# Kernel optimization log

Measured on AMD Instinct MI355X. Metric: run time of the kernel, lower is better.

## Reference

```python
import jax, jax.numpy as jnp
import numpy as np
from jax import lax

B, L, ENC_IN, MARK = 8, 512, 7, 4
D_MODEL, EXPAND, D_STATE, D_CONV = 512, 2, 16, 4
D_INNER = D_MODEL * EXPAND
DT_RANK = int(np.ceil(D_MODEL / 16))  # 32
PRED_LEN, C_OUT = 96, 7


def _positional_embedding(seq_len, d_model):
    pos = jnp.arange(seq_len, dtype=jnp.float32)[:, None]
    div = jnp.exp(jnp.arange(0, d_model, 2, dtype=jnp.float32) * (-np.log(10000.0) / d_model))
    pe = jnp.zeros((seq_len, d_model), dtype=jnp.float32)
    pe = pe.at[:, 0::2].set(jnp.sin(pos * div))
    pe = pe.at[:, 1::2].set(jnp.cos(pos * div))
    return pe  # [L, d_model]


def setup_inputs() -> dict:
    key = jax.random.key(0)
    ks = jax.random.split(key, 20)
    s = 0.02
    inp = {
        "x_enc": jax.random.normal(ks[0], (B, L, ENC_IN), jnp.float32),
        "x_mark_enc": jax.random.normal(ks[1], (B, L, MARK), jnp.float32),
        "x_dec": jax.random.normal(ks[2], (B, 144, ENC_IN), jnp.float32),
        "x_mark_dec": jax.random.normal(ks[3], (B, 144, MARK), jnp.float32),
        # DataEmbedding params
        "token_conv_w": jax.random.normal(ks[4], (D_MODEL, ENC_IN, 3), jnp.float32) * s,
        "temporal_w": jax.random.normal(ks[5], (D_MODEL, MARK), jnp.float32) * s,
        # Mamba params
        "in_proj_w": jax.random.normal(ks[6], (2 * D_INNER, D_MODEL), jnp.float32) * s,
        "conv1d_w": jax.random.normal(ks[7], (D_INNER, 1, D_CONV), jnp.float32) * s,
        "conv1d_b": jnp.zeros((D_INNER,), jnp.float32),
        "x_proj_w": jax.random.normal(ks[8], (DT_RANK + 2 * D_STATE, D_INNER), jnp.float32) * s,
        "dt_proj_w": jax.random.normal(ks[9], (D_INNER, DT_RANK), jnp.float32) * s,
        "dt_proj_b": jax.random.normal(ks[10], (D_INNER,), jnp.float32) * s,
        "A_log": jnp.log(jnp.broadcast_to(jnp.arange(1, D_STATE + 1, dtype=jnp.float32), (D_INNER, D_STATE))),
        "D_param": jnp.ones((D_INNER,), jnp.float32),
        "out_proj_w": jax.random.normal(ks[11], (D_MODEL, D_INNER), jnp.float32) * s,
        # prediction head
        "head_w": jax.random.normal(ks[12], (PRED_LEN * C_OUT, D_MODEL), jnp.float32) * s,
        "head_b": jnp.zeros((PRED_LEN * C_OUT,), jnp.float32),
    }
    return inp


def reference(x_enc, x_mark_enc, x_dec, x_mark_dec, token_conv_w, temporal_w,
              in_proj_w, conv1d_w, conv1d_b, x_proj_w, dt_proj_w, dt_proj_b,
              A_log, D_param, out_proj_w, head_w, head_b):
    # --- instance normalization (mean/std detached as in torch) ---
    mean_enc = lax.stop_gradient(jnp.mean(x_enc, axis=1, keepdims=True))       # [B,1,C]
    xc = x_enc - mean_enc
    std_enc = lax.stop_gradient(jnp.sqrt(jnp.var(xc, axis=1, keepdims=True) + 1e-5))
    xn = xc / std_enc                                                          # [B,L,C]

    # --- DataEmbedding: circular conv token emb + timeF linear + sinusoidal PE ---
    xp = jnp.pad(xn, ((0, 0), (1, 1), (0, 0)), mode="wrap")                    # circular pad on L
    val = lax.conv_general_dilated(xp.transpose(0, 2, 1), token_conv_w, (1,), "VALID")  # [B,D,L]
    val = val.transpose(0, 2, 1)                                               # [B,L,D]
    temp = x_mark_enc @ temporal_w.T                                           # [B,L,D]
    x = val + temp + _positional_embedding(L, D_MODEL)[None]                   # [B,L,D]

    # --- Mamba block ---
    xz = x @ in_proj_w.T                                                       # [B,L,2*Di]
    x_part, z = jnp.split(xz, 2, axis=-1)
    # causal depthwise conv over time
    xt = jnp.pad(x_part.transpose(0, 2, 1), ((0, 0), (0, 0), (D_CONV - 1, 0)))
    xconv = lax.conv_general_dilated(xt, conv1d_w, (1,), "VALID",
                                     feature_group_count=D_INNER) + conv1d_b[None, :, None]
    u = jax.nn.silu(xconv.transpose(0, 2, 1))                                  # [B,L,Di]

    dbl = u @ x_proj_w.T                                                       # [B,L,dt_rank+2n]
    dt_low = dbl[..., :DT_RANK]
    Bm = dbl[..., DT_RANK:DT_RANK + D_STATE]                                   # [B,L,n]
    Cm = dbl[..., DT_RANK + D_STATE:]                                          # [B,L,n]
    dt = jax.nn.softplus(dt_low @ dt_proj_w.T + dt_proj_b)                     # [B,L,Di]

    A = -jnp.exp(A_log)                                                        # [Di,n]
    deltaA = jnp.exp(dt[..., None] * A)                                        # [B,L,Di,n]
    deltaBu = dt[..., None] * Bm[:, :, None, :] * u[..., None]                 # [B,L,Di,n]

    def step(h, inputs):
        dA_t, dBu_t, c_t = inputs                                              # [B,Di,n],[B,Di,n],[B,n]
        h = dA_t * h + dBu_t
        y_t = jnp.einsum("bdn,bn->bd", h, c_t)
        return h, y_t

    h0 = jnp.zeros((B, D_INNER, D_STATE), dtype=x.dtype)
    _, ys = lax.scan(step, h0, (deltaA.transpose(1, 0, 2, 3),
                                deltaBu.transpose(1, 0, 2, 3),
                                Cm.transpose(1, 0, 2)))
    y = ys.transpose(1, 0, 2) + u * D_param                                    # [B,L,Di]
    y = y * jax.nn.silu(z)
    x_out = y @ out_proj_w.T                                                   # [B,L,D]

    # --- prediction head on last hidden state ---
    last = x_out[:, -1, :]                                                     # [B,D]
    pred = (last @ head_w.T + head_b).reshape(-1, PRED_LEN, C_OUT)
    return pred * std_enc + mean_enc
```

## Files before the change

### kernel.cpp

```cpp
#include <hip/hip_runtime.h>
#include <hip/hip_bf16.h>
#include <math.h>

#define BB 8
#define LL 512
#define CIN 7
#define MARKN 4
#define DM 512
#define DI 1024
#define NOUTC 672
#define NTC 16

typedef unsigned short ushortT;
typedef __attribute__((ext_vector_type(8))) short short8v;
typedef __attribute__((ext_vector_type(4))) float f32x4;

__device__ __forceinline__ float bf2f(ushortT u){ return __uint_as_float(((unsigned)u)<<16); }
__device__ __forceinline__ ushortT f2bf(float f){ __hip_bfloat16 h = __float2bfloat16(f); return *(ushortT*)&h; }

__global__ __launch_bounds__(512) void k_prep_embed(const float* __restrict__ xe,
    const float* __restrict__ xmark, const float* __restrict__ tw,
    const float* __restrict__ tpw, const float* __restrict__ inprojw,
    const float* __restrict__ xpw,
    __hip_bfloat16* __restrict__ xo, ushortT* __restrict__ wbf,
    ushortT* __restrict__ xpwbf, float* __restrict__ mean, float* __restrict__ stdv){
  __shared__ float sw[DM*21];
  __shared__ float sxr[10][CIN];
  __shared__ float smr[8][MARKN];
  __shared__ float sMean[8], sInv[8];
  int blk = blockIdx.x, tid = threadIdx.x;
  if(blk < 512){
    int b = blk >> 6;
    int l0 = (blk & 63) << 3;
    int wv = tid >> 6, t2 = tid & 63;
    if(wv < 7){
      int c = wv;
      const float* base = xe + (b*LL)*CIN + c;
      float v[8]; float s = 0.f;
      #pragma unroll
      for(int i=0;i<8;i++){ v[i] = base[(t2 + i*64)*CIN]; s += v[i]; }
      #pragma unroll
      for(int o=32;o>=1;o>>=1) s += __shfl_down(s, o);
      float m = __shfl(s, 0) * (1.0f/LL);
      float vs = 0.f;
      #pragma unroll
      for(int i=0;i<8;i++){ float dv = v[i]-m; vs += dv*dv; }
      #pragma unroll
      for(int o=32;o>=1;o>>=1) vs += __shfl_down(vs, o);
      float var = __shfl(vs, 0) * (1.0f/LL);
      float sd = sqrtf(var + 1e-5f);
      if(t2 == 0){
        sMean[c] = m; sInv[c] = 1.0f/sd;
        if(l0 == 0){ mean[b*CIN+c] = m; stdv[b*CIN+c] = sd; }
      }
    }
    __syncthreads();
    for(int i=tid; i<DM*21; i+=512) sw[i] = tw[i];
    if(tid < 70){
      int r = tid / CIN, c = tid % CIN;
      int ls = (l0 - 1 + r + LL) % LL;
      sxr[r][c] = (xe[(b*LL + ls)*CIN + c] - sMean[c]) * sInv[c];
    } else if(tid >= 128 && tid < 160){
      int i2 = tid - 128; int r = i2 >> 2, m = i2 & 3;
      smr[r][m] = xmark[(b*LL + l0 + r)*MARKN + m];
    }
    __syncthreads();
    int d = tid;
    float wv2[21];
    #pragma unroll
    for(int i=0;i<21;i++) wv2[i] = sw[d*21 + i];
    float tv[4];
    #pragma unroll
    for(int m=0;m<4;m++) tv[m] = tpw[d*MARKN + m];
    float divv = expf((float)(2*(d>>1)) * (-0.0179889460390159843f));
    bool isodd = (d & 1) != 0;
    #pragma unroll
    for(int ll=0; ll<8; ll++){
      float acc = 0.f;
      #pragma unroll
      for(int c=0;c<CIN;c++){
        #pragma unroll
        for(int k=0;k<3;k++) acc += sxr[ll+k][c] * wv2[c*3+k];
      }
      #pragma unroll
      for(int m=0;m<4;m++) acc += smr[ll][m] * tv[m];
      float ang = (float)(l0+ll) * divv;
      acc += isodd ? cosf(ang) : sinf(ang);
      xo[(size_t)(b*LL + l0 + ll)*DM + d] = __float2bfloat16(acc);
    }
  } else if(blk < 1024){
    int i = ((blk-512)*512 + tid)*4;
    float4 v = *(const float4*)(inprojw + i);
    ushort4 pk; pk.x=f2bf(v.x); pk.y=f2bf(v.y); pk.z=f2bf(v.z); pk.w=f2bf(v.w);
    *(ushort4*)(wbf + i) = pk;
  } else {
    int i = ((blk-1024)*512 + tid)*4;
    float4 v = *(const float4*)(xpw + i);
    ushort4 pk; pk.x=f2bf(v.x); pk.y=f2bf(v.y); pk.z=f2bf(v.z); pk.w=f2bf(v.w);
    *(ushort4*)(xpwbf + i) = pk;
  }
}

__global__ __launch_bounds__(256) void k_inproj_mfma(const ushortT* __restrict__ A,
    const ushortT* __restrict__ Bw, ushortT* __restrict__ C){
  __shared__ ushortT Asl[2][128*64];
  __shared__ ushortT Bsl[2][128*64];
  int tid = threadIdx.x;
  int w = tid >> 6, l = tid & 63;
  int m0 = blockIdx.y * 128, n0 = blockIdx.x * 128;
  int wr = w >> 1, wc = w & 1;
  f32x4 acc[4][4] = {};
  int srow = l >> 3;
  int scolswz = ((l & 7) * 16) ^ (srow << 4);

#define IP_STAGE(bufi, kt) do{ \
    _Pragma("unroll") \
    for(int i=0;i<4;i++){ \
      int r0 = w*32 + i*8; \
      int r = r0 + srow; \
      const ushortT* gA = A + (size_t)(m0 + r)*512 + (kt)*64 + (scolswz>>1); \
      const ushortT* gB = Bw + (size_t)(n0 + r)*512 + (kt)*64 + (scolswz>>1); \
      __builtin_amdgcn_global_load_lds( \
        (const __attribute__((address_space(1))) unsigned int*)(const void*)gA, \
        (__attribute__((address_space(3))) unsigned int*)(void*)(Asl[bufi] + r0*64), 16, 0, 0); \
      __builtin_amdgcn_global_load_lds( \
        (const __attribute__((address_space(1))) unsigned int*)(const void*)gB, \
        (__attribute__((address_space(3))) unsigned int*)(void*)(Bsl[bufi] + r0*64), 16, 0, 0); \
    } }while(0)

  IP_STAGE(0, 0);
  __syncthreads();
  int cur = 0;
  for(int kt = 0; kt < 8; ++kt){
    if(kt < 7) IP_STAGE(cur^1, kt+1);
    #pragma unroll
    for(int kk=0;kk<2;kk++){
      short8v af[4], bfr[4];
      int cb = kk*64 + (l>>4)*16;
      #pragma unroll
      for(int mf=0;mf<4;mf++){
        int ar = wr*64 + mf*16 + (l&15);
        af[mf] = *(const short8v*)(Asl[cur] + ar*64 + ((cb ^ ((ar&7)<<4))>>1));
      }
      #pragma unroll
      for(int nf=0;nf<4;nf++){
        int br = wc*64 + nf*16 + (l&15);
        bfr[nf] = *(const short8v*)(Bsl[cur] + br*64 + ((cb ^ ((br&7)<<4))>>1));
      }
      #pragma unroll
      for(int mf=0;mf<4;mf++)
        #pragma unroll
        for(int nf=0;nf<4;nf++)
          acc[mf][nf] = __builtin_amdgcn_mfma_f32_16x16x32_bf16(af[mf], bfr[nf], acc[mf][nf], 0, 0, 0);
    }
    __syncthreads();
    cur ^= 1;
  }
#undef IP_STAGE
  #pragma unroll
  for(int mf=0;mf<4;mf++){
    int rbase = m0 + wr*64 + mf*16 + (l>>4)*4;
    #pragma unroll
    for(int nf=0;nf<4;nf++){
      int col = n0 + wc*64 + nf*16 + (l&15);
      #pragma unroll
      for(int r=0;r<4;r++)
        C[(size_t)(rbase+r)*1024 + col] = f2bf(acc[mf][nf][r]);
    }
  }
}

__global__ __launch_bounds__(1024) void k_dwconv(const ushortT* __restrict__ xpbf,
    const float* __restrict__ cw, const float* __restrict__ cb,
    ushortT* __restrict__ ubf){
  int blk = blockIdx.x;
  int b = blk >> 5, l0 = (blk & 31) * 16;
  int d = threadIdx.x;
  const float4 w4 = *(const float4*)(cw + d*4);
  float bias = cb[d];
  const ushortT* base = xpbf + (size_t)(b*LL + l0)*1024 + d;
  float x0=0.f, x1=0.f, x2=0.f;
  if(l0 > 0){
    x0 = bf2f(base[-3*1024]); x1 = bf2f(base[-2*1024]); x2 = bf2f(base[-1*1024]);
  }
  #pragma unroll
  for(int ll=0; ll<16; ++ll){
    float x3 = bf2f(base[(size_t)ll*1024]);
    float acc = bias + x0*w4.x + x1*w4.y + x2*w4.z + x3*w4.w;
    float s = acc / (1.f + __expf(-acc));
    ubf[(size_t)(b*LL + l0 + ll)*1024 + d] = f2bf(s);
    x0 = x1; x1 = x2; x2 = x3;
  }
}

__global__ __launch_bounds__(256) void k_xproj_mfma(const ushortT* __restrict__ A,
    const ushortT* __restrict__ Bw, float* __restrict__ C){
  __shared__ ushortT Asl[2][32*64];
  __shared__ ushortT Bsl[2][64*64];
  int tid = threadIdx.x;
  int w = tid >> 6, l = tid & 63;
  int m0 = blockIdx.x * 32;
  f32x4 acc[2] = {};
  int srow = l >> 3;
  int scol = ((l & 7) * 16) ^ (srow << 4);

#define XP_STAGE(bufi, kt) do{ \
    { \
      int r0 = w*8; \
      const ushortT* gA = A + (size_t)(m0 + r0 + srow)*1024 + (kt)*64 + (scol>>1); \
      __builtin_amdgcn_global_load_lds( \
        (const __attribute__((address_space(1))) unsigned int*)(const void*)gA, \
        (__attribute__((address_space(3))) unsigned int*)(void*)(Asl[bufi] + r0*64), 16, 0, 0); \
    } \
    _Pragma("unroll") \
    for(int i=0;i<2;i++){ \
      int r0 = w*16 + i*8; \
      const ushortT* gB = Bw + (size_t)(r0 + srow)*1024 + (kt)*64 + (scol>>1); \
      __builtin_amdgcn_global_load_lds( \
        (const __attribute__((address_space(1))) unsigned int*)(const void*)gB, \
        (__attribute__((address_space(3))) unsigned int*)(void*)(Bsl[bufi] + r0*64), 16, 0, 0); \
    } }while(0)

  XP_STAGE(0, 0);
  __syncthreads();
  int cur = 0;
  for(int kt = 0; kt < 16; ++kt){
    if(kt < 15) XP_STAGE(cur^1, kt+1);
    #pragma unroll
    for(int kk=0;kk<2;kk++){
      int cb = kk*64 + (l>>4)*16;
      int ar = (w&1)*16 + (l&15);
      short8v af = *(const short8v*)(Asl[cur] + ar*64 + ((cb ^ ((ar&7)<<4))>>1));
      #pragma unroll
      for(int nf=0;nf<2;nf++){
        int br = (w>>1)*32 + nf*16 + (l&15);
        short8v bfv = *(const short8v*)(Bsl[cur] + br*64 + ((cb ^ ((br&7)<<4))>>1));
        acc[nf] = __builtin_amdgcn_mfma_f32_16x16x32_bf16(af, bfv, acc[nf], 0, 0, 0);
      }
    }
    __syncthreads();
    cur ^= 1;
  }
#undef XP_STAGE
  int rbase = m0 + (w&1)*16 + (l>>4)*4;
  #pragma unroll
  for(int nf=0;nf<2;nf++){
    int col = (w>>1)*32 + nf*16 + (l&15);
    #pragma unroll
    for(int r=0;r<4;r++)
      C[(size_t)(rbase+r)*64 + col] = acc[nf][r];
  }
}

__global__ __launch_bounds__(256) void k_scan_chunk(const float* __restrict__ dbl,
    const ushortT* __restrict__ ubf, const float* __restrict__ dtw,
    const float* __restrict__ dtb, const float* __restrict__ alog,
    float4* __restrict__ P4, float4* __restrict__ Q4){
  int tc = blockIdx.x;
  int dgrp = blockIdx.y;
  int b = blockIdx.z;
  int tid = threadIdx.x;
  int d = dgrp*256 + tid;
  __shared__ float sD[32][68];
  #pragma unroll
  for(int j=0;j<2;j++){
    int idx = j*256 + tid;
    int row = idx >> 4, q = idx & 15;
    float4 v = *(const float4*)(dbl + (size_t)(b*LL + tc*32 + row)*64 + q*4);
    *(float4*)(&sD[row][q*4]) = v;
  }
  float wdt[32];
  #pragma unroll
  for(int r4=0;r4<8;r4++){
    float4 v = *(const float4*)(dtw + (size_t)d*32 + r4*4);
    wdt[r4*4]=v.x; wdt[r4*4+1]=v.y; wdt[r4*4+2]=v.z; wdt[r4*4+3]=v.w;
  }
  float bias = dtb[d];
  float Ad[16];
  {
    float4 a0 = *(const float4*)(alog + d*16);
    float4 a1 = *(const float4*)(alog + d*16 + 4);
    float4 a2 = *(const float4*)(alog + d*16 + 8);
    float4 a3 = *(const float4*)(alog + d*16 + 12);
    Ad[0]=-__expf(a0.x); Ad[1]=-__expf(a0.y); Ad[2]=-__expf(a0.z); Ad[3]=-__expf(a0.w);
    Ad[4]=-__expf(a1.x); Ad[5]=-__expf(a1.y); Ad[6]=-__expf(a1.z); Ad[7]=-__expf(a1.w);
    Ad[8]=-__expf(a2.x); Ad[9]=-__expf(a2.y); Ad[10]=-__expf(a2.z); Ad[11]=-__expf(a2.w);
    Ad[12]=-__expf(a3.x); Ad[13]=-__expf(a3.y); Ad[14]=-__expf(a3.z); Ad[15]=-__expf(a3.w);
  }
  __syncthreads();
  float h[16];
  #pragma unroll
  for(int n=0;n<16;n++) h[n] = 0.f;
  float Ss = 0.f;
  const ushortT* up = ubf + (size_t)(b*LL + tc*32)*1024 + d;
  #pragma unroll 2
  for(int t=0;t<32;t++){
    float a2 = bias;
    #pragma unroll
    for(int r=0;r<32;r++) a2 += sD[t][r]*wdt[r];
    float dtv = (a2 > 20.f) ? a2 : __logf(1.f + __expf(a2));
    float uv = bf2f(up[(size_t)t*1024]);
    float wt = dtv * uv;
    Ss += dtv;
    #pragma unroll
    for(int n=0;n<16;n++){
      float e = __expf(dtv * Ad[n]);
      h[n] = h[n]*e + wt*sD[t][32+n];
    }
  }
  size_t base4 = (size_t)(tc*8 + b)*4*1024 + d;
  #pragma unroll
  for(int n4=0;n4<4;n4++){
    Q4[base4 + n4*1024] = make_float4(h[n4*4], h[n4*4+1], h[n4*4+2], h[n4*4+3]);
    P4[base4 + n4*1024] = make_float4(__expf(Ss*Ad[n4*4]), __expf(Ss*Ad[n4*4+1]),
                                      __expf(Ss*Ad[n4*4+2]), __expf(Ss*Ad[n4*4+3]));
  }
}

__global__ __launch_bounds__(256) void k_scan_combine(const float4* __restrict__ P4,
    const float4* __restrict__ Q4, const float* __restrict__ dbl,
    const ushortT* __restrict__ ubf, const ushortT* __restrict__ xbf,
    const ushortT* __restrict__ wbf, const float* __restrict__ Dp,
    float* __restrict__ yv){
  int tid = threadIdx.x;
  int unit = blockIdx.x*64 + (tid>>2);
  int sub = tid & 3;
  int b = unit >> 10, d = unit & 1023;
  const ushortT* xr = xbf + (size_t)(b*LL + LL-1)*512 + sub*128;
  const ushortT* wr = wbf + (size_t)(1024 + d)*512 + sub*128;
  float zl = 0.f;
  #pragma unroll
  for(int k=0;k<128;k+=8){
    short8v xv = *(const short8v*)(xr + k);
    short8v wv = *(const short8v*)(wr + k);
    #pragma unroll
    for(int j=0;j<8;j++) zl += bf2f((ushortT)xv[j])*bf2f((ushortT)wv[j]);
  }
  zl += __shfl_xor(zl, 1);
  zl += __shfl_xor(zl, 2);
  float h0=0.f, h1=0.f, h2=0.f, h3=0.f;
  #pragma unroll
  for(int c=0;c<NTC;c++){
    size_t idx = (size_t)(c*8 + b)*4*1024 + sub*1024 + d;
    float4 pv = P4[idx];
    float4 qv = Q4[idx];
    h0 = pv.x*h0 + qv.x;
    h1 = pv.y*h1 + qv.y;
    h2 = pv.z*h2 + qv.z;
    h3 = pv.w*h3 + qv.w;
  }
  const float* Crow = dbl + (size_t)(b*LL + LL-1)*64 + 48 + sub*4;
  float y = Crow[0]*h0 + Crow[1]*h1 + Crow[2]*h2 + Crow[3]*h3;
  y += __shfl_xor(y, 1);
  y += __shfl_xor(y, 2);
  if(sub == 0){
    float ul = bf2f(ubf[(size_t)(b*LL + LL-1)*1024 + d]);
    float sz = zl / (1.f + __expf(-zl));
    yv[b*1024 + d] = (y + ul*Dp[d]) * sz;
  }
}

__global__ __launch_bounds__(256) void k_outproj(const float* __restrict__ yv,
    const float* __restrict__ W, float* __restrict__ xout){
  int tid = threadIdx.x;
  int j = blockIdx.x*8 + (tid>>5);
  int ks = tid & 31;
  float a[8] = {};
  #pragma unroll
  for(int t=0;t<8;t++){
    int k = ks*4 + t*128;
    float4 wv = *(const float4*)(W + (size_t)j*1024 + k);
    #pragma unroll
    for(int b=0;b<8;b++){
      float4 xv = *(const float4*)(yv + b*1024 + k);
      a[b] += xv.x*wv.x + xv.y*wv.y + xv.z*wv.z + xv.w*wv.w;
    }
  }
  #pragma unroll
  for(int b=0;b<8;b++){
    #pragma unroll
    for(int o=16;o>=1;o>>=1) a[b] += __shfl_xor(a[b], o);
  }
  if(ks==0){
    #pragma unroll
    for(int b=0;b<8;b++) xout[b*512 + j] = a[b];
  }
}

__global__ __launch_bounds__(256) void k_head(const float* __restrict__ xout,
    const float* __restrict__ W, const float* __restrict__ hb,
    const float* __restrict__ mean, const float* __restrict__ stdv,
    float* __restrict__ out){
  int tid = threadIdx.x;
  int o = blockIdx.x*8 + (tid>>5);
  int ks = tid & 31;
  float a[8] = {};
  #pragma unroll
  for(int t=0;t<4;t++){
    int k = ks*4 + t*128;
    float4 wv = *(const float4*)(W + (size_t)o*512 + k);
    #pragma unroll
    for(int b=0;b<8;b++){
      float4 xv = *(const float4*)(xout + b*512 + k);
      a[b] += xv.x*wv.x + xv.y*wv.y + xv.z*wv.z + xv.w*wv.w;
    }
  }
  #pragma unroll
  for(int b=0;b<8;b++){
    #pragma unroll
    for(int oo=16;oo>=1;oo>>=1) a[b] += __shfl_xor(a[b], oo);
  }
  if(ks==0){
    int c = o % 7;
    #pragma unroll
    for(int b=0;b<8;b++){
      float v = a[b] + hb[o];
      out[b*NOUTC + o] = v * stdv[b*CIN + c] + mean[b*CIN + c];
    }
  }
}

extern "C" void kernel_launch(void* const* d_in, const int* in_sizes, int n_in,
                              void* d_out, int out_size, void* d_ws, size_t ws_size,
                              hipStream_t stream) {
  const float* x_enc   = (const float*)d_in[0];
  const float* x_mark  = (const float*)d_in[1];
  const float* tconvw  = (const float*)d_in[4];
  const float* tempw   = (const float*)d_in[5];
  const float* inprojw = (const float*)d_in[6];
  const float* convw   = (const float*)d_in[7];
  const float* convb   = (const float*)d_in[8];
  const float* xprojw  = (const float*)d_in[9];
  const float* dtw     = (const float*)d_in[10];
  const float* dtb     = (const float*)d_in[11];
  const float* alog    = (const float*)d_in[12];
  const float* dpar    = (const float*)d_in[13];
  const float* outw    = (const float*)d_in[14];
  const float* headw   = (const float*)d_in[15];
  const float* headb   = (const float*)d_in[16];

  float* ws    = (float*)d_ws;
  float* mean  = ws;
  float* stdv  = ws + 64;
  ushortT* xbf = (ushortT*)(ws + 128);
  ushortT* wbf = (ushortT*)(ws + 1048704);
  ushortT* xpwbf=(ushortT*)(ws + 1572992);
  ushortT* xpbf= (ushortT*)(ws + 1605760);
  ushortT* ubf = (ushortT*)(ws + 3702912);
  float* dbl   = ws + 5800064;
  float4* P4   = (float4*)(ws + 6062208);
  float4* Q4   = (float4*)(ws + 8159360);
  float* yv    = ws + 10256512;
  float* xout  = ws + 10264704;
  float* out   = (float*)d_out;

  k_prep_embed<<<1056, 512, 0, stream>>>(x_enc, x_mark, tconvw, tempw, inprojw, xprojw,
                                         (__hip_bfloat16*)xbf, wbf, xpwbf, mean, stdv);
  k_inproj_mfma<<<dim3(8, 32), 256, 0, stream>>>(xbf, wbf, xpbf);
  k_dwconv<<<256, 1024, 0, stream>>>(xpbf, convw, convb, ubf);
  k_xproj_mfma<<<128, 256, 0, stream>>>(ubf, xpwbf, dbl);
  k_scan_chunk<<<dim3(NTC, 4, 8), 256, 0, stream>>>(dbl, ubf, dtw, dtb, alog, P4, Q4);
  k_scan_combine<<<128, 256, 0, stream>>>(P4, Q4, dbl, ubf, xbf, wbf, dpar, yv);
  k_outproj<<<64, 256, 0, stream>>>(yv, outw, xout);
  k_head  <<<84, 256, 0, stream>>>(xout, headw, headb, mean, stdv, out);
}
```

Before: 88.84 us.

## Fuse x_proj GEMM into chunked scan kernel via shared memory

Merges the x_proj MFMA GEMM and the chunk scan into one kernel. Each block (chunk, batch) with 1024 threads has its first 4 waves compute the 32x64 dbl tile into LDS, then all threads run the scan for their channel. The last C row is exported separately for the combine step. This removes a launch and the global round trip of dbl. The cost is that 12 of 16 waves sit idle during the GEMM, and the grid shrinks to 128 large blocks, which may lower occupancy for the scan.

```diff
diff --git a/kernel.cpp b/kernel.cpp
--- a/kernel.cpp
+++ b/kernel.cpp
@@ -193,82 +193,74 @@
   }
 }
 
-__global__ __launch_bounds__(256) void k_xproj_mfma(const ushortT* __restrict__ A,
-    const ushortT* __restrict__ Bw, float* __restrict__ C){
+__global__ __launch_bounds__(1024) void k_xscan(const ushortT* __restrict__ Aub,
+    const ushortT* __restrict__ Bw, const float* __restrict__ dtw,
+    const float* __restrict__ dtb, const float* __restrict__ alog,
+    float4* __restrict__ P4, float4* __restrict__ Q4, float* __restrict__ Crow){
+  int tc = blockIdx.x, b = blockIdx.y;
+  int tid = threadIdx.x;
   __shared__ ushortT Asl[2][32*64];
   __shared__ ushortT Bsl[2][64*64];
-  int tid = threadIdx.x;
-  int w = tid >> 6, l = tid & 63;
-  int m0 = blockIdx.x * 32;
+  __shared__ float sD[32][68];
+  int m0g = b*LL + tc*32;
   f32x4 acc[2] = {};
+  int w2 = (tid >> 6) & 3, l = tid & 63;
   int srow = l >> 3;
   int scol = ((l & 7) * 16) ^ (srow << 4);
-
-#define XP_STAGE(bufi, kt) do{ \
+  bool mfw = tid < 256;
+
+#define XS_STAGE(bufi, kt) do{ \
     { \
-      int r0 = w*8; \
-      const ushortT* gA = A + (size_t)(m0 + r0 + srow)*1024 + (kt)*64 + (scol>>1); \
+      int r0 = w2*8; \
+      const ushortT* gA = Aub + (size_t)(m0g + r0 + srow)*1024 + (kt)*64 + (scol>>1); \
       __builtin_amdgcn_global_load_lds( \
         (const __attribute__((address_space(1))) unsigned int*)(const void*)gA, \
         (__attribute__((address_space(3))) unsigned int*)(void*)(Asl[bufi] + r0*64), 16, 0, 0); \
     } \
     _Pragma("unroll") \
     for(int i=0;i<2;i++){ \
-      int r0 = w*16 + i*8; \
+      int r0 = w2*16 + i*8; \
       const ushortT* gB = Bw + (size_t)(r0 + srow)*1024 + (kt)*64 + (scol>>1); \
       __builtin_amdgcn_global_load_lds( \
         (const __attribute__((address_space(1))) unsigned int*)(const void*)gB, \
         (__attribute__((address_space(3))) unsigned int*)(void*)(Bsl[bufi] + r0*64), 16, 0, 0); \
     } }while(0)
 
-  XP_STAGE(0, 0);
+  if(mfw) XS_STAGE(0, 0);
   __syncthreads();
   int cur = 0;
   for(int kt = 0; kt < 16; ++kt){
-    if(kt < 15) XP_STAGE(cur^1, kt+1);
-    #pragma unroll
-    for(int kk=0;kk<2;kk++){
-      int cb = kk*64 + (l>>4)*16;
-      int ar = (w&1)*16 + (l&15);
-      short8v af = *(const short8v*)(Asl[cur] + ar*64 + ((cb ^ ((ar&7)<<4))>>1));
-      #pragma unroll
-      for(int nf=0;nf<2;nf++){
-        int br = (w>>1)*32 + nf*16 + (l&15);
-        short8v bfv = *(const short8v*)(Bsl[cur] + br*64 + ((cb ^ ((br&7)<<4))>>1));
-        acc[nf] = __builtin_amdgcn_mfma_f32_16x16x32_bf16(af, bfv, acc[nf], 0, 0, 0);
+    if(mfw){
+      if(kt < 15) XS_STAGE(cur^1, kt+1);
+      #pragma unroll
+      for(int kk=0;kk<2;kk++){
+        int cb = kk*64 + (l>>4)*16;
+        int ar = (w2&1)*16 + (l&15);
+        short8v af = *(const short8v*)(Asl[cur] + ar*64 + ((cb ^ ((ar&7)<<4))>>1));
+        #pragma unroll
+        for(int nf=0;nf<2;nf++){
+          int br = (w2>>1)*32 + nf*16 + (l&15);
+          short8v bfv = *(const short8v*)(Bsl[cur] + br*64 + ((cb ^ ((br&7)<<4))>>1));
+          acc[nf] = __builtin_amdgcn_mfma_f32_16x16x32_bf16(af, bfv, acc[nf], 0, 0, 0);
+        }
       }
     }
     __syncthreads();
     cur ^= 1;
   }
-#undef XP_STAGE
-  int rbase = m0 + (w&1)*16 + (l>>4)*4;
-  #pragma unroll
-  for(int nf=0;nf<2;nf++){
-    int col = (w>>1)*32 + nf*16 + (l&15);
-    #pragma unroll
-    for(int r=0;r<4;r++)
-      C[(size_t)(rbase+r)*64 + col] = acc[nf][r];
-  }
-}
-
-__global__ __launch_bounds__(256) void k_scan_chunk(const float* __restrict__ dbl,
-    const ushortT* __restrict__ ubf, const float* __restrict__ dtw,
-    const float* __restrict__ dtb, const float* __restrict__ alog,
-    float4* __restrict__ P4, float4* __restrict__ Q4){
-  int tc = blockIdx.x;
-  int dgrp = blockIdx.y;
-  int b = blockIdx.z;
-  int tid = threadIdx.x;
-  int d = dgrp*256 + tid;
-  __shared__ float sD[32][68];
-  #pragma unroll
-  for(int j=0;j<2;j++){
-    int idx = j*256 + tid;
-    int row = idx >> 4, q = idx & 15;
-    float4 v = *(const float4*)(dbl + (size_t)(b*LL + tc*32 + row)*64 + q*4);
-    *(float4*)(&sD[row][q*4]) = v;
-  }
+#undef XS_STAGE
+  if(mfw){
+    int rbase = (w2&1)*16 + (l>>4)*4;
+    #pragma unroll
+    for(int nf=0;nf<2;nf++){
+      int colx = (w2>>1)*32 + nf*16 + (l&15);
+      #pragma unroll
+      for(int r=0;r<4;r++) sD[rbase+r][colx] = acc[nf][r];
+    }
+  }
+  __syncthreads();
+  if(tc == 15 && tid < 16) Crow[b*16 + tid] = sD[31][48 + tid];
+  int d = tid;
   float wdt[32];
   #pragma unroll
   for(int r4=0;r4<8;r4++){
@@ -287,12 +279,11 @@
     Ad[8]=-__expf(a2.x); Ad[9]=-__expf(a2.y); Ad[10]=-__expf(a2.z); Ad[11]=-__expf(a2.w);
     Ad[12]=-__expf(a3.x); Ad[13]=-__expf(a3.y); Ad[14]=-__expf(a3.z); Ad[15]=-__expf(a3.w);
   }
-  __syncthreads();
   float h[16];
   #pragma unroll
   for(int n=0;n<16;n++) h[n] = 0.f;
   float Ss = 0.f;
-  const ushortT* up = ubf + (size_t)(b*LL + tc*32)*1024 + d;
+  const ushortT* up = Aub + (size_t)m0g*1024 + d;
   #pragma unroll 2
   for(int t=0;t<32;t++){
     float a2 = bias;
@@ -318,7 +309,7 @@
 }
 
 __global__ __launch_bounds__(256) void k_scan_combine(const float4* __restrict__ P4,
-    const float4* __restrict__ Q4, const float* __restrict__ dbl,
+    const float4* __restrict__ Q4, const float* __restrict__ Crow,
     const ushortT* __restrict__ ubf, const ushortT* __restrict__ xbf,
     const ushortT* __restrict__ wbf, const float* __restrict__ Dp,
     float* __restrict__ yv){
@@ -349,8 +340,8 @@
     h2 = pv.z*h2 + qv.z;
     h3 = pv.w*h3 + qv.w;
   }
-  const float* Crow = dbl + (size_t)(b*LL + LL-1)*64 + 48 + sub*4;
-  float y = Crow[0]*h0 + Crow[1]*h1 + Crow[2]*h2 + Crow[3]*h3;
+  const float* Cr = Crow + b*16 + sub*4;
+  float y = Cr[0]*h0 + Cr[1]*h1 + Cr[2]*h2 + Cr[3]*h3;
   y += __shfl_xor(y, 1);
   y += __shfl_xor(y, 2);
   if(sub == 0){
@@ -447,20 +438,19 @@
   ushortT* xpwbf=(ushortT*)(ws + 1572992);
   ushortT* xpbf= (ushortT*)(ws + 1605760);
   ushortT* ubf = (ushortT*)(ws + 3702912);
-  float* dbl   = ws + 5800064;
-  float4* P4   = (float4*)(ws + 6062208);
-  float4* Q4   = (float4*)(ws + 8159360);
-  float* yv    = ws + 10256512;
-  float* xout  = ws + 10264704;
+  float4* P4   = (float4*)(ws + 5800064);
+  float4* Q4   = (float4*)(ws + 7897216);
+  float* yv    = ws + 9994368;
+  float* xout  = ws + 10002560;
+  float* Crow  = ws + 10006656;
   float* out   = (float*)d_out;
 
   k_prep_embed<<<1056, 512, 0, stream>>>(x_enc, x_mark, tconvw, tempw, inprojw, xprojw,
                                          (__hip_bfloat16*)xbf, wbf, xpwbf, mean, stdv);
   k_inproj_mfma<<<dim3(8, 32), 256, 0, stream>>>(xbf, wbf, xpbf);
   k_dwconv<<<256, 1024, 0, stream>>>(xpbf, convw, convb, ubf);
-  k_xproj_mfma<<<128, 256, 0, stream>>>(ubf, xpwbf, dbl);
-  k_scan_chunk<<<dim3(NTC, 4, 8), 256, 0, stream>>>(dbl, ubf, dtw, dtb, alog, P4, Q4);
-  k_scan_combine<<<128, 256, 0, stream>>>(P4, Q4, dbl, ubf, xbf, wbf, dpar, yv);
+  k_xscan<<<dim3(NTC, 8), 1024, 0, stream>>>(ubf, xpwbf, dtw, dtb, alog, P4, Q4, Crow);
+  k_scan_combine<<<128, 256, 0, stream>>>(P4, Q4, Crow, ubf, xbf, wbf, dpar, yv);
   k_outproj<<<64, 256, 0, stream>>>(yv, outw, xout);
   k_head  <<<84, 256, 0, stream>>>(xout, headw, headb, mean, stdv, out);
 }
```

Result: slower. 98.99 us (+11.4%).

## Fuse depthwise causal conv and SiLU into in_proj GEMM epilogue with halo rows

Applied to the files above, without the earlier changes.

The in_proj GEMM now also computes 16 halo rows above each 128-row tile, so the causal depthwise conv plus SiLU can run directly from LDS in the epilogue. This removes the separate dwconv kernel launch and the global write and re-read of the bf16 x-projection intermediate. The cost is redundant halo MFMA work in two waves and a larger LDS footprint. The epilogue conv loop is also serialised at 64 rows per thread.

```diff
diff --git a/kernel.cpp b/kernel.cpp
--- a/kernel.cpp
+++ b/kernel.cpp
@@ -101,96 +101,117 @@
   }
 }
 
-__global__ __launch_bounds__(256) void k_inproj_mfma(const ushortT* __restrict__ A,
-    const ushortT* __restrict__ Bw, ushortT* __restrict__ C){
-  __shared__ ushortT Asl[2][128*64];
-  __shared__ ushortT Bsl[2][128*64];
+__global__ __launch_bounds__(256) void k_inproj_dw(const ushortT* __restrict__ A,
+    const ushortT* __restrict__ Bw, const float* __restrict__ cw,
+    const float* __restrict__ cb, ushortT* __restrict__ ubf){
+  __shared__ __align__(16) ushortT LDSI[2*144*64 + 2*128*64];
+#define ASLB(bufi) (LDSI + (bufi)*144*64)
+#define BSLB(bufi) (LDSI + 2*144*64 + (bufi)*128*64)
   int tid = threadIdx.x;
   int w = tid >> 6, l = tid & 63;
   int m0 = blockIdx.y * 128, n0 = blockIdx.x * 128;
   int wr = w >> 1, wc = w & 1;
+  int hbase = (m0 == 0) ? 0 : m0 - 16;
   f32x4 acc[4][4] = {};
+  f32x4 hacc[4] = {};
   int srow = l >> 3;
   int scolswz = ((l & 7) * 16) ^ (srow << 4);
 
-#define IP_STAGE(bufi, kt) do{ \
+#define IPD_STAGE(bufi, kt) do{ \
     _Pragma("unroll") \
     for(int i=0;i<4;i++){ \
       int r0 = w*32 + i*8; \
-      int r = r0 + srow; \
-      const ushortT* gA = A + (size_t)(m0 + r)*512 + (kt)*64 + (scolswz>>1); \
-      const ushortT* gB = Bw + (size_t)(n0 + r)*512 + (kt)*64 + (scolswz>>1); \
+      const ushortT* gA = A + (size_t)(m0 + r0 + srow)*512 + (kt)*64 + (scolswz>>1); \
+      const ushortT* gB = Bw + (size_t)(n0 + r0 + srow)*512 + (kt)*64 + (scolswz>>1); \
       __builtin_amdgcn_global_load_lds( \
         (const __attribute__((address_space(1))) unsigned int*)(const void*)gA, \
-        (__attribute__((address_space(3))) unsigned int*)(void*)(Asl[bufi] + r0*64), 16, 0, 0); \
+        (__attribute__((address_space(3))) unsigned int*)(void*)(ASLB(bufi) + (16 + r0)*64), 16, 0, 0); \
       __builtin_amdgcn_global_load_lds( \
         (const __attribute__((address_space(1))) unsigned int*)(const void*)gB, \
-        (__attribute__((address_space(3))) unsigned int*)(void*)(Bsl[bufi] + r0*64), 16, 0, 0); \
+        (__attribute__((address_space(3))) unsigned int*)(void*)(BSLB(bufi) + r0*64), 16, 0, 0); \
+    } \
+    if(w < 2){ \
+      int hr0 = w*8; \
+      const ushortT* gH = A + (size_t)(hbase + hr0 + srow)*512 + (kt)*64 + (scolswz>>1); \
+      __builtin_amdgcn_global_load_lds( \
+        (const __attribute__((address_space(1))) unsigned int*)(const void*)gH, \
+        (__attribute__((address_space(3))) unsigned int*)(void*)(ASLB(bufi) + hr0*64), 16, 0, 0); \
     } }while(0)
 
-  IP_STAGE(0, 0);
+  IPD_STAGE(0, 0);
   __syncthreads();
   int cur = 0;
   for(int kt = 0; kt < 8; ++kt){
-    if(kt < 7) IP_STAGE(cur^1, kt+1);
+    if(kt < 7) IPD_STAGE(cur^1, kt+1);
     #pragma unroll
     for(int kk=0;kk<2;kk++){
       short8v af[4], bfr[4];
-      int cb = kk*64 + (l>>4)*16;
+      int cb2 = kk*64 + (l>>4)*16;
       #pragma unroll
       for(int mf=0;mf<4;mf++){
-        int ar = wr*64 + mf*16 + (l&15);
-        af[mf] = *(const short8v*)(Asl[cur] + ar*64 + ((cb ^ ((ar&7)<<4))>>1));
+        int ar = 16 + wr*64 + mf*16 + (l&15);
+        af[mf] = *(const short8v*)(ASLB(cur) + ar*64 + ((cb2 ^ ((ar&7)<<4))>>1));
       }
       #pragma unroll
       for(int nf=0;nf<4;nf++){
         int br = wc*64 + nf*16 + (l&15);
-        bfr[nf] = *(const short8v*)(Bsl[cur] + br*64 + ((cb ^ ((br&7)<<4))>>1));
+        bfr[nf] = *(const short8v*)(BSLB(cur) + br*64 + ((cb2 ^ ((br&7)<<4))>>1));
       }
       #pragma unroll
       for(int mf=0;mf<4;mf++)
         #pragma unroll
         for(int nf=0;nf<4;nf++)
           acc[mf][nf] = __builtin_amdgcn_mfma_f32_16x16x32_bf16(af[mf], bfr[nf], acc[mf][nf], 0, 0, 0);
+      if(w < 2){
+        int har = (l&15);
+        short8v haf = *(const short8v*)(ASLB(cur) + har*64 + ((cb2 ^ ((har&7)<<4))>>1));
+        #pragma unroll
+        for(int nf=0;nf<4;nf++)
+          hacc[nf] = __builtin_amdgcn_mfma_f32_16x16x32_bf16(haf, bfr[nf], hacc[nf], 0, 0, 0);
+      }
     }
     __syncthreads();
     cur ^= 1;
   }
-#undef IP_STAGE
+#undef IPD_STAGE
+  ushortT* sU = LDSI;
+  const int US = 136;
   #pragma unroll
   for(int mf=0;mf<4;mf++){
-    int rbase = m0 + wr*64 + mf*16 + (l>>4)*4;
+    int rb = 16 + wr*64 + mf*16 + (l>>4)*4;
     #pragma unroll
     for(int nf=0;nf<4;nf++){
-      int col = n0 + wc*64 + nf*16 + (l&15);
-      #pragma unroll
-      for(int r=0;r<4;r++)
-        C[(size_t)(rbase+r)*1024 + col] = f2bf(acc[mf][nf][r]);
-    }
-  }
-}
-
-__global__ __launch_bounds__(1024) void k_dwconv(const ushortT* __restrict__ xpbf,
-    const float* __restrict__ cw, const float* __restrict__ cb,
-    ushortT* __restrict__ ubf){
-  int blk = blockIdx.x;
-  int b = blk >> 5, l0 = (blk & 31) * 16;
-  int d = threadIdx.x;
-  const float4 w4 = *(const float4*)(cw + d*4);
-  float bias = cb[d];
-  const ushortT* base = xpbf + (size_t)(b*LL + l0)*1024 + d;
-  float x0=0.f, x1=0.f, x2=0.f;
-  if(l0 > 0){
-    x0 = bf2f(base[-3*1024]); x1 = bf2f(base[-2*1024]); x2 = bf2f(base[-1*1024]);
-  }
-  #pragma unroll
-  for(int ll=0; ll<16; ++ll){
-    float x3 = bf2f(base[(size_t)ll*1024]);
-    float acc = bias + x0*w4.x + x1*w4.y + x2*w4.z + x3*w4.w;
-    float s = acc / (1.f + __expf(-acc));
-    ubf[(size_t)(b*LL + l0 + ll)*1024 + d] = f2bf(s);
-    x0 = x1; x1 = x2; x2 = x3;
-  }
+      int col = wc*64 + nf*16 + (l&15);
+      #pragma unroll
+      for(int r=0;r<4;r++) sU[(rb+r)*US + col] = f2bf(acc[mf][nf][r]);
+    }
+  }
+  if(w < 2){
+    int rb = (l>>4)*4;
+    #pragma unroll
+    for(int nf=0;nf<4;nf++){
+      int col = wc*64 + nf*16 + (l&15);
+      #pragma unroll
+      for(int r=0;r<4;r++) sU[(rb+r)*US + col] = f2bf(hacc[nf][r]);
+    }
+  }
+  __syncthreads();
+  int col = tid & 127, rh = tid >> 7;
+  const float4 w4 = *(const float4*)(cw + (size_t)(n0+col)*4);
+  float bias = cb[n0+col];
+  int lbase = m0 & 511;
+  for(int R = rh*64; R < rh*64 + 64; ++R){
+    int lg = lbase + R;
+    float x3 = bf2f(sU[(16+R)*US + col]);
+    float x2 = (lg>=1) ? bf2f(sU[(15+R)*US + col]) : 0.f;
+    float x1 = (lg>=2) ? bf2f(sU[(14+R)*US + col]) : 0.f;
+    float x0 = (lg>=3) ? bf2f(sU[(13+R)*US + col]) : 0.f;
+    float a = bias + x0*w4.x + x1*w4.y + x2*w4.z + x3*w4.w;
+    float s = a / (1.f + __expf(-a));
+    ubf[(size_t)(m0+R)*1024 + n0 + col] = f2bf(s);
+  }
+#undef ASLB
+#undef BSLB
 }
 
 __global__ __launch_bounds__(256) void k_xproj_mfma(const ushortT* __restrict__ A,
@@ -445,19 +466,17 @@
   ushortT* xbf = (ushortT*)(ws + 128);
   ushortT* wbf = (ushortT*)(ws + 1048704);
   ushortT* xpwbf=(ushortT*)(ws + 1572992);
-  ushortT* xpbf= (ushortT*)(ws + 1605760);
-  ushortT* ubf = (ushortT*)(ws + 3702912);
-  float* dbl   = ws + 5800064;
-  float4* P4   = (float4*)(ws + 6062208);
-  float4* Q4   = (float4*)(ws + 8159360);
-  float* yv    = ws + 10256512;
-  float* xout  = ws + 10264704;
+  ushortT* ubf = (ushortT*)(ws + 1605760);
+  float* dbl   = ws + 3702912;
+  float4* P4   = (float4*)(ws + 3965056);
+  float4* Q4   = (float4*)(ws + 6062208);
+  float* yv    = ws + 8159360;
+  float* xout  = ws + 8167552;
   float* out   = (float*)d_out;
 
   k_prep_embed<<<1056, 512, 0, stream>>>(x_enc, x_mark, tconvw, tempw, inprojw, xprojw,
                                          (__hip_bfloat16*)xbf, wbf, xpwbf, mean, stdv);
-  k_inproj_mfma<<<dim3(8, 32), 256, 0, stream>>>(xbf, wbf, xpbf);
-  k_dwconv<<<256, 1024, 0, stream>>>(xpbf, convw, convb, ubf);
+  k_inproj_dw<<<dim3(8, 32), 256, 0, stream>>>(xbf, wbf, convw, convb, ubf);
   k_xproj_mfma<<<128, 256, 0, stream>>>(ubf, xpwbf, dbl);
   k_scan_chunk<<<dim3(NTC, 4, 8), 256, 0, stream>>>(dbl, ubf, dtw, dtb, alog, P4, Q4);
   k_scan_combine<<<128, 256, 0, stream>>>(P4, Q4, dbl, ubf, xbf, wbf, dpar, yv);
```

Result: slower. 97.09 us (+9.3%).
